# Kernel optimization log

Measured on AMD Instinct MI355X. Metric: run time of the kernel, lower is better.

## Reference

```python
import jax, jax.numpy as jnp
import numpy as np

DIM = 256
N = 8192

def setup_inputs() -> dict:
    key = jax.random.key(0)
    kx, kq, kk, kv = jax.random.split(key, 4)
    X = jax.random.normal(kx, (N, DIM), dtype=jnp.float32)
    # nn.Linear weights are [out, in]; xavier-uniform-like scale via normal/sqrt(dim)
    Wq = jax.random.normal(kq, (DIM, DIM), dtype=jnp.float32) / np.sqrt(DIM)
    Wk = jax.random.normal(kk, (DIM, DIM), dtype=jnp.float32) / np.sqrt(DIM)
    Wv = jax.random.normal(kv, (DIM, DIM), dtype=jnp.float32) / np.sqrt(DIM)
    return {"X": X, "Wq": Wq, "Wk": Wk, "Wv": Wv}

def reference(X, Wq, Wk, Wv):
    # nn.Linear(no bias): y = X @ W.T
    Q = X @ Wq.T  # [N, D]
    K = X @ Wk.T
    V = X @ Wv.T
    scores = (Q @ K.T) / jnp.sqrt(jnp.asarray(DIM, dtype=X.dtype))  # [N, N]
    softed = jax.nn.softmax(scores, axis=-1)
    return softed @ V  # [N, D]
```

## Files before the change

### kernel.cpp

```cpp
#include <hip/hip_runtime.h>
#include <math.h>

#define N 8192
#define D 256
#define QBLK 128
#define KBLK 32

typedef float f32x4 __attribute__((ext_vector_type(4)));
typedef short bf16x8 __attribute__((ext_vector_type(8)));

#define MFMA(a, b, c) __builtin_amdgcn_mfma_f32_16x16x32_bf16((a), (b), (c), 0, 0, 0)
#define BAR() __builtin_amdgcn_s_barrier()

__device__ __forceinline__ unsigned short f2b(float f) {
    unsigned u = __builtin_bit_cast(unsigned, f);
    u = u + 0x7fffu + ((u >> 16) & 1u);
    return (unsigned short)(u >> 16);
}
__device__ __forceinline__ unsigned pk2(float a, float b) {
    return (unsigned)f2b(a) | ((unsigned)f2b(b) << 16);
}
__device__ __forceinline__ unsigned cvtpk(float a, float b) {
    unsigned r;
    asm("v_cvt_pk_bf16_f32 %0, %1, %2" : "=v"(r) : "v"(a), "v"(b));
    return r;
}
__device__ __forceinline__ float b2f(short s) {
    unsigned x = ((unsigned)(unsigned short)s) << 16;
    return __builtin_bit_cast(float, x);
}

__global__ __launch_bounds__(256) void proj_mfma(
    const float* __restrict__ X, const float* __restrict__ Wq,
    const float* __restrict__ Wk, const float* __restrict__ Wv,
    unsigned short* __restrict__ Qb, unsigned short* __restrict__ Kb,
    unsigned short* __restrict__ Vt)
{
    __shared__ char Wl[32768];
    const int z = blockIdx.z;
    const float* W = (z == 0) ? Wq : (z == 1) ? Wk : Wv;
    const int r0 = blockIdx.x * 64;
    const int c0 = blockIdx.y * 64;
    const int t = threadIdx.x, w = t >> 6, l = t & 63;
    const int lo = l & 15, hi = l >> 4;

    #pragma unroll
    for (int i = 0; i < 16; ++i) {
        int e4 = t + i * 256;
        int col = e4 >> 6, kk4 = e4 & 63;
        float4 f = *(const float4*)&W[(size_t)(c0 + col) * D + kk4 * 4];
        unsigned long long v = (unsigned long long)pk2(f.x, f.y)
                             | ((unsigned long long)pk2(f.z, f.w) << 32);
        *(unsigned long long*)(Wl + col * 512 + ((kk4 * 8) ^ ((col & 7) << 4))) = v;
    }
    __syncthreads();

    bf16x8 xf[8];
    {
        const float* xr = X + (size_t)(r0 + w * 16 + lo) * D;
        #pragma unroll
        for (int ks = 0; ks < 8; ++ks) {
            float4 a = *(const float4*)(xr + ks * 32 + hi * 8);
            float4 b = *(const float4*)(xr + ks * 32 + hi * 8 + 4);
            bf16x8 v;
            v[0] = (short)f2b(a.x); v[1] = (short)f2b(a.y);
            v[2] = (short)f2b(a.z); v[3] = (short)f2b(a.w);
            v[4] = (short)f2b(b.x); v[5] = (short)f2b(b.y);
            v[6] = (short)f2b(b.z); v[7] = (short)f2b(b.w);
            xf[ks] = v;
        }
    }

    f32x4 acc[4];
    #pragma unroll
    for (int nc = 0; nc < 4; ++nc) acc[nc] = (f32x4){0.f, 0.f, 0.f, 0.f};
    #pragma unroll
    for (int ks = 0; ks < 8; ++ks) {
        #pragma unroll
        for (int nc = 0; nc < 4; ++nc) {
            int col = nc * 16 + lo;
            bf16x8 wf = *(const bf16x8*)(Wl + col * 512 +
                                         ((ks * 64 + hi * 16) ^ ((col & 7) << 4)));
            acc[nc] = MFMA(xf[ks], wf, acc[nc]);
        }
    }

    if (z < 2) {
        unsigned short* Y = z ? Kb : Qb;
        #pragma unroll
        for (int nc = 0; nc < 4; ++nc)
            #pragma unroll
            for (int r = 0; r < 4; ++r)
                Y[(size_t)(r0 + w * 16 + hi * 4 + r) * D + c0 + nc * 16 + lo] = f2b(acc[nc][r]);
    } else {
        #pragma unroll
        for (int nc = 0; nc < 4; ++nc) {
            unsigned long long v = (unsigned long long)pk2(acc[nc][0], acc[nc][1])
                                 | ((unsigned long long)pk2(acc[nc][2], acc[nc][3]) << 32);
            *(unsigned long long*)&Vt[(size_t)(c0 + nc * 16 + lo) * N + r0 + w * 16 + hi * 4] = v;
        }
    }
}

__device__ __forceinline__ void stage_tile4(
    const unsigned short* __restrict__ Kb, const unsigned short* __restrict__ Vt,
    char* kbuf, char* vbuf, int kt, int t)
{
    #pragma unroll
    for (int i = 0; i < 4; ++i) {
        int c = t + i * 256;
        {
            int row = c >> 5, xc = c & 31;
            int pk = (((row >> 2) & 3) << 3) | (((row >> 4) & 1) << 2) | (row & 3);
            const unsigned short* gp = Kb + (size_t)(kt + pk) * D + (xc ^ (row & 7)) * 8;
            __builtin_amdgcn_global_load_lds(
                (const __attribute__((address_space(1))) void*)gp,
                (__attribute__((address_space(3))) void*)(kbuf + c * 16), 16, 0, 0);
        }
        {
            int dd = c >> 2, xc = c & 3;
            const unsigned short* gp = Vt + (size_t)dd * N + kt + xc * 8;
            __builtin_amdgcn_global_load_lds(
                (const __attribute__((address_space(1))) void*)gp,
                (__attribute__((address_space(3))) void*)(vbuf + c * 16), 16, 0, 0);
        }
    }
}

template <int KSPLIT>
__global__ __launch_bounds__(256, 2) void attn_mfma(
    const unsigned short* __restrict__ Qb,
    const unsigned short* __restrict__ Kb,
    const unsigned short* __restrict__ Vt,
    unsigned short* __restrict__ Opart,
    float2* __restrict__ ml)
{
    extern __shared__ char smem[];
    const int t = threadIdx.x;
    const int w = t >> 6;
    const int l = t & 63;
    const int lo = l & 15;
    const int hi = l >> 4;
    const int bid = blockIdx.x;
    const int split = bid % KSPLIT;
    const int xblk = bid / KSPLIT;
    const int q0 = xblk * QBLK + w * 32;
    const int kbase = split * (N / KSPLIT);
    const int NTS = N / KSPLIT / KBLK;

    bf16x8 qf[2][8];
    #pragma unroll
    for (int s = 0; s < 2; ++s) {
        const unsigned short* qrow = Qb + (size_t)(q0 + s * 16 + lo) * D;
        #pragma unroll
        for (int ks = 0; ks < 8; ++ks)
            qf[s][ks] = *(const bf16x8*)(qrow + ks * 32 + hi * 8);
    }

    stage_tile4(Kb, Vt, smem, smem + 32768, kbase, t);
    stage_tile4(Kb, Vt, smem + 16384, smem + 32768 + 16384, kbase + KBLK, t);

    f32x4 Oacc[2][16];
    #pragma unroll
    for (int s = 0; s < 2; ++s)
        #pragma unroll
        for (int i = 0; i < 16; ++i) Oacc[s][i] = (f32x4){0.f, 0.f, 0.f, 0.f};
    float m_run[2] = {-INFINITY, -INFINITY};
    float l_run[2] = {0.f, 0.f};
    const float scale2 = 0.09016994f;

    asm volatile("s_waitcnt vmcnt(8)" ::: "memory");
    BAR();

    for (int tt = 0; tt < NTS; ++tt) {
        const int cur = tt & 1;
        const char* Kl = smem + cur * 16384;
        const char* Vl = smem + 32768 + cur * 16384;

        f32x4 sacc[2][2];
        #pragma unroll
        for (int s = 0; s < 2; ++s)
            #pragma unroll
            for (int kg = 0; kg < 2; ++kg) sacc[s][kg] = (f32x4){0.f, 0.f, 0.f, 0.f};
        __builtin_amdgcn_s_setprio(1);
        #pragma unroll
        for (int ks = 0; ks < 8; ++ks) {
            #pragma unroll
            for (int kg = 0; kg < 2; ++kg) {
                int key = kg * 16 + lo;
                bf16x8 kf = *(const bf16x8*)(Kl + key * 512 +
                                             ((ks * 64 + hi * 16) ^ ((key & 7) << 4)));
                sacc[0][kg] = MFMA(kf, qf[0][ks], sacc[0][kg]);
                sacc[1][kg] = MFMA(kf, qf[1][ks], sacc[1][kg]);
            }
        }
        __builtin_amdgcn_s_setprio(0);

        float mx[2];
        #pragma unroll
        for (int s = 0; s < 2; ++s) {
            float m = -INFINITY;
            #pragma unroll
            for (int kg = 0; kg < 2; ++kg)
                #pragma unroll
                for (int r = 0; r < 4; ++r) m = fmaxf(m, sacc[s][kg][r]);
            mx[s] = m * scale2;
        }

        bool need = (mx[0] > m_run[0] + 11.0f) || (mx[1] > m_run[1] + 11.0f);
        if (__builtin_expect(__any(need), 0)) {
            #pragma unroll
            for (int s = 0; s < 2; ++s) {
                float m = mx[s];
                m = fmaxf(m, __shfl_xor(m, 16));
                m = fmaxf(m, __shfl_xor(m, 32));
                float m_new = fmaxf(m_run[s], m);
                float corr = exp2f(m_run[s] - m_new);
                m_run[s] = m_new;
                l_run[s] *= corr;
                float cr0 = __shfl(corr, hi * 4 + 0);
                float cr1 = __shfl(corr, hi * 4 + 1);
                float cr2 = __shfl(corr, hi * 4 + 2);
                float cr3 = __shfl(corr, hi * 4 + 3);
                #pragma unroll
                for (int nc = 0; nc < 16; ++nc) {
                    Oacc[s][nc][0] *= cr0; Oacc[s][nc][1] *= cr1;
                    Oacc[s][nc][2] *= cr2; Oacc[s][nc][3] *= cr3;
                }
            }
        }

        bf16x8 pa[2];
        float ts[2];
        #pragma unroll
        for (int s = 0; s < 2; ++s) {
            float p[8];
            float sum = 0.f;
            #pragma unroll
            for (int kg = 0; kg < 2; ++kg)
                #pragma unroll
                for (int r = 0; r < 4; ++r) {
                    float pv = exp2f(sacc[s][kg][r] * scale2 - m_run[s]);
                    p[kg * 4 + r] = pv;
                    sum += pv;
                }
            ts[s] = sum;
            union { unsigned u[4]; bf16x8 v; } u0;
            #pragma unroll
            for (int j = 0; j < 4; ++j)
                u0.u[j] = cvtpk(p[j * 2], p[j * 2 + 1]);
            pa[s] = u0.v;
        }

        __builtin_amdgcn_s_setprio(1);
        #pragma unroll
        for (int nc = 0; nc < 16; ++nc) {
            int dd = nc * 16 + lo;
            bf16x8 v0 = *(const bf16x8*)(Vl + dd * 64 + hi * 16);
            Oacc[0][nc] = MFMA(pa[0], v0, Oacc[0][nc]);
            Oacc[1][nc] = MFMA(pa[1], v0, Oacc[1][nc]);
        }
        __builtin_amdgcn_s_setprio(0);

        l_run[0] += ts[0];
        l_run[1] += ts[1];

        asm volatile("" ::: "memory");
        BAR();
        if (tt + 2 < NTS) {
            stage_tile4(Kb, Vt, smem + cur * 16384, smem + 32768 + cur * 16384,
                        kbase + (tt + 2) * KBLK, t);
            asm volatile("s_waitcnt vmcnt(8)" ::: "memory");
            BAR();
        } else if (tt + 1 < NTS) {
            asm volatile("s_waitcnt vmcnt(0)" ::: "memory");
            BAR();
        }
    }

    #pragma unroll
    for (int s = 0; s < 2; ++s) {
        l_run[s] += __shfl_xor(l_run[s], 16);
        l_run[s] += __shfl_xor(l_run[s], 32);
    }
    #pragma unroll
    for (int s = 0; s < 2; ++s) {
        const int qrow = q0 + s * 16 + hi * 4;
        #pragma unroll
        for (int nc = 0; nc < 16; ++nc)
            #pragma unroll
            for (int r = 0; r < 4; ++r)
                Opart[((size_t)split * N + qrow + r) * D + nc * 16 + lo] = f2b(Oacc[s][nc][r]);
        if (hi == 0)
            ml[(size_t)split * N + q0 + s * 16 + lo] = make_float2(m_run[s], l_run[s]);
    }
}

__global__ __launch_bounds__(256) void combine_kernel(
    const unsigned short* __restrict__ Opart, const float2* __restrict__ ml,
    float* __restrict__ out, int nsplit)
{
    int idx = blockIdx.x * 256 + threadIdx.x;
    int q = idx >> 5;
    int d0 = (idx & 31) * 8;

    float M = -INFINITY;
    for (int i = 0; i < nsplit; ++i) M = fmaxf(M, ml[(size_t)i * N + q].x);
    float L = 0.f;
    float acc[8] = {};
    for (int i = 0; i < nsplit; ++i) {
        float2 v = ml[(size_t)i * N + q];
        float wgt = exp2f(v.x - M);
        L += wgt * v.y;
        bf16x8 ov = *(const bf16x8*)&Opart[((size_t)i * N + q) * D + d0];
        #pragma unroll
        for (int j = 0; j < 8; ++j) acc[j] += wgt * b2f(ov[j]);
    }
    float r = 1.f / L;
    #pragma unroll
    for (int j = 0; j < 8; ++j) out[(size_t)q * D + d0 + j] = acc[j] * r;
}

extern "C" void kernel_launch(void* const* d_in, const int* in_sizes, int n_in,
                              void* d_out, int out_size, void* d_ws, size_t ws_size,
                              hipStream_t stream) {
    const float* X  = (const float*)d_in[0];
    const float* Wq = (const float*)d_in[1];
    const float* Wk = (const float*)d_in[2];
    const float* Wv = (const float*)d_in[3];

    unsigned short* ws = (unsigned short*)d_ws;
    const size_t ndq = (size_t)N * D;
    unsigned short* Qb = ws;
    unsigned short* Kb = ws + ndq;
    unsigned short* Vt = ws + 2 * ndq;
    unsigned short* Opart = ws + 3 * ndq;

    auto need = [ndq](int ks) {
        return (size_t)(3 + ks) * ndq * 2 + (size_t)ks * N * 8;
    };
    const int ksplit = (ws_size >= need(8)) ? 8 : (ws_size >= need(4)) ? 4 : 2;
    float2* ml = (float2*)(ws + (3 + ksplit) * ndq);

    (void)hipFuncSetAttribute((const void*)attn_mfma<8>,
                              hipFuncAttributeMaxDynamicSharedMemorySize, 65536);
    (void)hipFuncSetAttribute((const void*)attn_mfma<4>,
                              hipFuncAttributeMaxDynamicSharedMemorySize, 65536);
    (void)hipFuncSetAttribute((const void*)attn_mfma<2>,
                              hipFuncAttributeMaxDynamicSharedMemorySize, 65536);

    proj_mfma<<<dim3(N / 64, D / 64, 3), 256, 0, stream>>>(X, Wq, Wk, Wv, Qb, Kb, Vt);
    if (ksplit == 8)
        attn_mfma<8><<<dim3((N / QBLK) * 8), 256, 65536, stream>>>(Qb, Kb, Vt, Opart, ml);
    else if (ksplit == 4)
        attn_mfma<4><<<dim3((N / QBLK) * 4), 256, 65536, stream>>>(Qb, Kb, Vt, Opart, ml);
    else
        attn_mfma<2><<<dim3((N / QBLK) * 2), 256, 65536, stream>>>(Qb, Kb, Vt, Opart, ml);
    combine_kernel<<<(N * D / 8) / 256, 256, 0, stream>>>(Opart, ml, (float*)d_out, ksplit);
}
```

Before: 118.1 us.

## Switch attention inner loop to 32x32x16 MFMA with split K/V staging

Rewrites the attention kernel to use 32x32x16 bf16 MFMA instructions, so each wave owns 32 query rows in one accumulator set. The output is computed transposed so that each lane holds a single query row, which removes the per-row correction shuffles in the online softmax. K and V staging are split so that the K refill is issued right after the QK MFMAs and the V refill after the PV MFMAs, and the V tile gets an XOR swizzle against LDS bank conflicts. Each block also starts its key-tile loop at a rotated offset to spread memory accesses across blocks, and outputs are written as packed 64-bit stores. In exchange there are more barriers per iteration and the register allocation changes under the 2-block occupancy bound.

Measured after the change: 127.7 us. 8.1% more time.

```diff
diff --git a/kernel.cpp b/kernel.cpp
--- a/kernel.cpp
+++ b/kernel.cpp
@@ -7,10 +7,13 @@
 #define KBLK 32
 
 typedef float f32x4 __attribute__((ext_vector_type(4)));
+typedef float f32x16 __attribute__((ext_vector_type(16)));
 typedef short bf16x8 __attribute__((ext_vector_type(8)));
 
-#define MFMA(a, b, c) __builtin_amdgcn_mfma_f32_16x16x32_bf16((a), (b), (c), 0, 0, 0)
+#define MFMA16(a, b, c) __builtin_amdgcn_mfma_f32_16x16x32_bf16((a), (b), (c), 0, 0, 0)
+#define MFMA32(a, b, c) __builtin_amdgcn_mfma_f32_32x32x16_bf16((a), (b), (c), 0, 0, 0)
 #define BAR() __builtin_amdgcn_s_barrier()
+#define CFENCE() asm volatile("" ::: "memory")
 
 __device__ __forceinline__ unsigned short f2b(float f) {
     unsigned u = __builtin_bit_cast(unsigned, f);
@@ -81,7 +84,7 @@
             int col = nc * 16 + lo;
             bf16x8 wf = *(const bf16x8*)(Wl + col * 512 +
                                          ((ks * 64 + hi * 16) ^ ((col & 7) << 4)));
-            acc[nc] = MFMA(xf[ks], wf, acc[nc]);
+            acc[nc] = MFMA16(xf[ks], wf, acc[nc]);
         }
     }
 
@@ -102,28 +105,31 @@
     }
 }
 
-__device__ __forceinline__ void stage_tile4(
-    const unsigned short* __restrict__ Kb, const unsigned short* __restrict__ Vt,
-    char* kbuf, char* vbuf, int kt, int t)
+__device__ __forceinline__ void stage_K(const unsigned short* __restrict__ Kb,
+                                        char* kbuf, int kt, int t)
 {
     #pragma unroll
     for (int i = 0; i < 4; ++i) {
         int c = t + i * 256;
-        {
-            int row = c >> 5, xc = c & 31;
-            int pk = (((row >> 2) & 3) << 3) | (((row >> 4) & 1) << 2) | (row & 3);
-            const unsigned short* gp = Kb + (size_t)(kt + pk) * D + (xc ^ (row & 7)) * 8;
-            __builtin_amdgcn_global_load_lds(
-                (const __attribute__((address_space(1))) void*)gp,
-                (__attribute__((address_space(3))) void*)(kbuf + c * 16), 16, 0, 0);
-        }
-        {
-            int dd = c >> 2, xc = c & 3;
-            const unsigned short* gp = Vt + (size_t)dd * N + kt + xc * 8;
-            __builtin_amdgcn_global_load_lds(
-                (const __attribute__((address_space(1))) void*)gp,
-                (__attribute__((address_space(3))) void*)(vbuf + c * 16), 16, 0, 0);
-        }
+        int r = c >> 5, xc = c & 31;
+        int pk = (r & 0x13) | ((r & 4) << 1) | ((r & 8) >> 1);
+        const unsigned short* gp = Kb + (size_t)(kt + pk) * D + (xc ^ (r & 7)) * 8;
+        __builtin_amdgcn_global_load_lds(
+            (const __attribute__((address_space(1))) void*)gp,
+            (__attribute__((address_space(3))) void*)(kbuf + c * 16), 16, 0, 0);
+    }
+}
+__device__ __forceinline__ void stage_V(const unsigned short* __restrict__ Vt,
+                                        char* vbuf, int kt, int t)
+{
+    #pragma unroll
+    for (int i = 0; i < 4; ++i) {
+        int c = t + i * 256;
+        int dd = c >> 2, xc = c & 3;
+        const unsigned short* gp = Vt + (size_t)dd * N + kt + (xc ^ (dd & 3)) * 8;
+        __builtin_amdgcn_global_load_lds(
+            (const __attribute__((address_space(1))) void*)gp,
+            (__attribute__((address_space(3))) void*)(vbuf + c * 16), 16, 0, 0);
     }
 }
 
@@ -139,34 +145,35 @@
     const int t = threadIdx.x;
     const int w = t >> 6;
     const int l = t & 63;
-    const int lo = l & 15;
-    const int hi = l >> 4;
+    const int r = l & 31;
+    const int hi1 = l >> 5;
     const int bid = blockIdx.x;
     const int split = bid % KSPLIT;
     const int xblk = bid / KSPLIT;
     const int q0 = xblk * QBLK + w * 32;
     const int kbase = split * (N / KSPLIT);
     const int NTS = N / KSPLIT / KBLK;
-
-    bf16x8 qf[2][8];
-    #pragma unroll
-    for (int s = 0; s < 2; ++s) {
-        const unsigned short* qrow = Qb + (size_t)(q0 + s * 16 + lo) * D;
-        #pragma unroll
-        for (int ks = 0; ks < 8; ++ks)
-            qf[s][ks] = *(const bf16x8*)(qrow + ks * 32 + hi * 8);
-    }
-
-    stage_tile4(Kb, Vt, smem, smem + 32768, kbase, t);
-    stage_tile4(Kb, Vt, smem + 16384, smem + 32768 + 16384, kbase + KBLK, t);
-
-    f32x4 Oacc[2][16];
-    #pragma unroll
-    for (int s = 0; s < 2; ++s)
-        #pragma unroll
-        for (int i = 0; i < 16; ++i) Oacc[s][i] = (f32x4){0.f, 0.f, 0.f, 0.f};
-    float m_run[2] = {-INFINITY, -INFINITY};
-    float l_run[2] = {0.f, 0.f};
+    const int p0 = bid & (NTS - 1);
+
+    bf16x8 qf[16];
+    {
+        const unsigned short* qrow = Qb + (size_t)(q0 + r) * D;
+        #pragma unroll
+        for (int ks = 0; ks < 16; ++ks)
+            qf[ks] = *(const bf16x8*)(qrow + ks * 16 + hi1 * 8);
+    }
+
+    stage_K(Kb, smem,         kbase + p0 * KBLK, t);
+    stage_V(Vt, smem + 32768, kbase + p0 * KBLK, t);
+    stage_K(Kb, smem + 16384,         kbase + ((p0 + 1) & (NTS - 1)) * KBLK, t);
+    stage_V(Vt, smem + 32768 + 16384, kbase + ((p0 + 1) & (NTS - 1)) * KBLK, t);
+
+    f32x16 Oacc[8];
+    #pragma unroll
+    for (int nc = 0; nc < 8; ++nc)
+        #pragma unroll
+        for (int e = 0; e < 16; ++e) Oacc[nc][e] = 0.f;
+    float m_run = -INFINITY, l_run = 0.f;
     const float scale2 = 0.09016994f;
 
     asm volatile("s_waitcnt vmcnt(8)" ::: "memory");
@@ -174,126 +181,95 @@
 
     for (int tt = 0; tt < NTS; ++tt) {
         const int cur = tt & 1;
-        const char* Kl = smem + cur * 16384;
-        const char* Vl = smem + 32768 + cur * 16384;
-
-        f32x4 sacc[2][2];
-        #pragma unroll
-        for (int s = 0; s < 2; ++s)
+        char* Kl = smem + cur * 16384;
+        char* Vl = smem + 32768 + cur * 16384;
+
+        f32x16 sacc;
+        #pragma unroll
+        for (int e = 0; e < 16; ++e) sacc[e] = 0.f;
+        __builtin_amdgcn_s_setprio(1);
+        #pragma unroll
+        for (int ks = 0; ks < 16; ++ks) {
+            bf16x8 kf = *(const bf16x8*)(Kl + r * 512 + (((ks * 2 + hi1) ^ (r & 7)) * 16));
+            sacc = MFMA32(kf, qf[ks], sacc);
+        }
+        __builtin_amdgcn_s_setprio(0);
+
+        if (tt + 2 < NTS) {
+            CFENCE(); BAR(); CFENCE();
+            stage_K(Kb, Kl, kbase + ((p0 + tt + 2) & (NTS - 1)) * KBLK, t);
+        }
+
+        float m0 = fmaxf(fmaxf(sacc[0], sacc[1]),   fmaxf(sacc[2], sacc[3]));
+        float m1 = fmaxf(fmaxf(sacc[4], sacc[5]),   fmaxf(sacc[6], sacc[7]));
+        float m2 = fmaxf(fmaxf(sacc[8], sacc[9]),   fmaxf(sacc[10], sacc[11]));
+        float m3 = fmaxf(fmaxf(sacc[12], sacc[13]), fmaxf(sacc[14], sacc[15]));
+        float pm = fmaxf(fmaxf(m0, m1), fmaxf(m2, m3)) * scale2;
+
+        bool need = pm > m_run + 11.0f;
+        if (__builtin_expect(__any(need), 0)) {
+            float m2x = fmaxf(pm, __shfl_xor(pm, 32));
+            float m_new = fmaxf(m_run, m2x);
+            float corr = exp2f(m_run - m_new);
+            m_run = m_new;
+            l_run *= corr;
             #pragma unroll
-            for (int kg = 0; kg < 2; ++kg) sacc[s][kg] = (f32x4){0.f, 0.f, 0.f, 0.f};
+            for (int nc = 0; nc < 8; ++nc)
+                #pragma unroll
+                for (int e = 0; e < 16; ++e) Oacc[nc][e] *= corr;
+        }
+
+        bf16x8 pb[2];
+        float sum = 0.f;
+        #pragma unroll
+        for (int s1 = 0; s1 < 2; ++s1) {
+            union { unsigned u[4]; bf16x8 v; } uu;
+            #pragma unroll
+            for (int j2 = 0; j2 < 4; ++j2) {
+                float a = exp2f(sacc[s1 * 8 + j2 * 2]     * scale2 - m_run);
+                float b = exp2f(sacc[s1 * 8 + j2 * 2 + 1] * scale2 - m_run);
+                sum += a + b;
+                uu.u[j2] = cvtpk(a, b);
+            }
+            pb[s1] = uu.v;
+        }
+        l_run += sum;
+
         __builtin_amdgcn_s_setprio(1);
         #pragma unroll
-        for (int ks = 0; ks < 8; ++ks) {
-            #pragma unroll
-            for (int kg = 0; kg < 2; ++kg) {
-                int key = kg * 16 + lo;
-                bf16x8 kf = *(const bf16x8*)(Kl + key * 512 +
-                                             ((ks * 64 + hi * 16) ^ ((key & 7) << 4)));
-                sacc[0][kg] = MFMA(kf, qf[0][ks], sacc[0][kg]);
-                sacc[1][kg] = MFMA(kf, qf[1][ks], sacc[1][kg]);
-            }
+        for (int nc = 0; nc < 8; ++nc) {
+            const char* vrow = Vl + (nc * 32 + r) * 64;
+            bf16x8 va0 = *(const bf16x8*)(vrow + ((hi1       ^ (r & 3)) * 16));
+            bf16x8 va1 = *(const bf16x8*)(vrow + (((2 + hi1) ^ (r & 3)) * 16));
+            Oacc[nc] = MFMA32(va0, pb[0], Oacc[nc]);
+            Oacc[nc] = MFMA32(va1, pb[1], Oacc[nc]);
         }
         __builtin_amdgcn_s_setprio(0);
 
-        float mx[2];
-        #pragma unroll
-        for (int s = 0; s < 2; ++s) {
-            float m = -INFINITY;
-            #pragma unroll
-            for (int kg = 0; kg < 2; ++kg)
-                #pragma unroll
-                for (int r = 0; r < 4; ++r) m = fmaxf(m, sacc[s][kg][r]);
-            mx[s] = m * scale2;
-        }
-
-        bool need = (mx[0] > m_run[0] + 11.0f) || (mx[1] > m_run[1] + 11.0f);
-        if (__builtin_expect(__any(need), 0)) {
-            #pragma unroll
-            for (int s = 0; s < 2; ++s) {
-                float m = mx[s];
-                m = fmaxf(m, __shfl_xor(m, 16));
-                m = fmaxf(m, __shfl_xor(m, 32));
-                float m_new = fmaxf(m_run[s], m);
-                float corr = exp2f(m_run[s] - m_new);
-                m_run[s] = m_new;
-                l_run[s] *= corr;
-                float cr0 = __shfl(corr, hi * 4 + 0);
-                float cr1 = __shfl(corr, hi * 4 + 1);
-                float cr2 = __shfl(corr, hi * 4 + 2);
-                float cr3 = __shfl(corr, hi * 4 + 3);
-                #pragma unroll
-                for (int nc = 0; nc < 16; ++nc) {
-                    Oacc[s][nc][0] *= cr0; Oacc[s][nc][1] *= cr1;
-                    Oacc[s][nc][2] *= cr2; Oacc[s][nc][3] *= cr3;
-                }
-            }
-        }
-
-        bf16x8 pa[2];
-        float ts[2];
-        #pragma unroll
-        for (int s = 0; s < 2; ++s) {
-            float p[8];
-            float sum = 0.f;
-            #pragma unroll
-            for (int kg = 0; kg < 2; ++kg)
-                #pragma unroll
-                for (int r = 0; r < 4; ++r) {
-                    float pv = exp2f(sacc[s][kg][r] * scale2 - m_run[s]);
-                    p[kg * 4 + r] = pv;
-                    sum += pv;
-                }
-            ts[s] = sum;
-            union { unsigned u[4]; bf16x8 v; } u0;
-            #pragma unroll
-            for (int j = 0; j < 4; ++j)
-                u0.u[j] = cvtpk(p[j * 2], p[j * 2 + 1]);
-            pa[s] = u0.v;
-        }
-
-        __builtin_amdgcn_s_setprio(1);
-        #pragma unroll
-        for (int nc = 0; nc < 16; ++nc) {
-            int dd = nc * 16 + lo;
-            bf16x8 v0 = *(const bf16x8*)(Vl + dd * 64 + hi * 16);
-            Oacc[0][nc] = MFMA(pa[0], v0, Oacc[0][nc]);
-            Oacc[1][nc] = MFMA(pa[1], v0, Oacc[1][nc]);
-        }
-        __builtin_amdgcn_s_setprio(0);
-
-        l_run[0] += ts[0];
-        l_run[1] += ts[1];
-
-        asm volatile("" ::: "memory");
-        BAR();
         if (tt + 2 < NTS) {
-            stage_tile4(Kb, Vt, smem + cur * 16384, smem + 32768 + cur * 16384,
-                        kbase + (tt + 2) * KBLK, t);
+            CFENCE(); BAR(); CFENCE();
+            stage_V(Vt, Vl, kbase + ((p0 + tt + 2) & (NTS - 1)) * KBLK, t);
             asm volatile("s_waitcnt vmcnt(8)" ::: "memory");
-            BAR();
+            BAR(); CFENCE();
         } else if (tt + 1 < NTS) {
             asm volatile("s_waitcnt vmcnt(0)" ::: "memory");
-            BAR();
-        }
-    }
-
-    #pragma unroll
-    for (int s = 0; s < 2; ++s) {
-        l_run[s] += __shfl_xor(l_run[s], 16);
-        l_run[s] += __shfl_xor(l_run[s], 32);
-    }
-    #pragma unroll
-    for (int s = 0; s < 2; ++s) {
-        const int qrow = q0 + s * 16 + hi * 4;
-        #pragma unroll
-        for (int nc = 0; nc < 16; ++nc)
-            #pragma unroll
-            for (int r = 0; r < 4; ++r)
-                Opart[((size_t)split * N + qrow + r) * D + nc * 16 + lo] = f2b(Oacc[s][nc][r]);
-        if (hi == 0)
-            ml[(size_t)split * N + q0 + s * 16 + lo] = make_float2(m_run[s], l_run[s]);
-    }
+            BAR(); CFENCE();
+        }
+    }
+
+    l_run += __shfl_xor(l_run, 32);
+    const size_t orow = ((size_t)split * N + q0 + r) * D;
+    #pragma unroll
+    for (int nc = 0; nc < 8; ++nc)
+        #pragma unroll
+        for (int g = 0; g < 4; ++g) {
+            unsigned long long v =
+                  (unsigned long long)pk2(Oacc[nc][g * 4 + 0], Oacc[nc][g * 4 + 1])
+                | ((unsigned long long)pk2(Oacc[nc][g * 4 + 2], Oacc[nc][g * 4 + 3]) << 32);
+            *(unsigned long long*)&Opart[orow + nc * 32 + g * 8 + hi1 * 4] = v;
+        }
+    if (l < 32)
+        ml[(size_t)split * N + q0 + r] = make_float2(m_run, l_run);
 }
 
 __global__ __launch_bounds__(256) void combine_kernel(
```
